# Optimization experiments

Measured on AMD Instinct MI355X. Metric: run time of the kernel, lower is better.

The kernel has to match this reference:

```python
import jax, jax.numpy as jnp
import numpy as np


def _sobel_kernels():
    # Stack the four fixed 3x3 operators into one [4,1,3,3] OIHW kernel so
    # the four single-channel convs become a single 4-output-channel conv.
    f_x = [[-1, -2, -1], [0, 0, 0], [1, 2, 1]]
    f_y = [[-1, 0, 1], [-2, 0, 2], [-1, 0, 1]]
    f_tl_br = [[-2, -1, 0], [-1, 0, 1], [0, 1, 2]]
    f_tr_bl = [[0, -1, -2], [1, 0, -1], [2, 1, 0]]
    k = np.stack([f_x, f_y, f_tl_br, f_tr_bl]).astype(np.float32)  # [4,3,3]
    return jnp.asarray(k[:, None, :, :])  # [4,1,3,3]


def setup_inputs() -> dict:
    key = jax.random.key(0)
    lab = jax.random.normal(key, (64, 1, 512, 512), dtype=jnp.float32)
    return {"lab": lab, "kernels": _sobel_kernels()}


def reference(lab, kernels):
    # lab: [B,1,H,W]; kernels: [4,1,3,3]
    lab_l = lab.astype(jnp.float32)
    taps = jax.lax.conv_general_dilated(
        lab_l, kernels,
        window_strides=(1, 1), padding=((1, 1), (1, 1)),
        dimension_numbers=("NCHW", "OIHW", "NCHW"))  # [B,4,H,W]
    edge = jnp.sum(jnp.abs(taps), axis=1)  # [B,H,W]
    # edge[edge > 0] = 1 then .long(); abs-sum is >= 0 so this is a 0/1 map
    edge = jnp.where(edge > 0, 1, 0).astype(jnp.int32)
    return edge  # squeezed: channel dim already reduced
```

## Files before the change

kernel.cpp:

```cpp
#include <hip/hip_runtime.h>


#define IMG_W 512
#define IMG_H 512
#define TROWS 16
#define SROWS (TROWS + 2)

struct Row {
  float4 lo, hi;
  float lft, rgt;
};

__device__ __forceinline__ float rget(const Row& r, int k) {
  switch (k) {
    case 0: return r.lft;
    case 1: return r.lo.x; case 2: return r.lo.y;
    case 3: return r.lo.z; case 4: return r.lo.w;
    case 5: return r.hi.x; case 6: return r.hi.y;
    case 7: return r.hi.z; case 8: return r.hi.w;
    default: return r.rgt;
  }
}

__device__ __forceinline__ void compute_store(const Row& T, const Row& M,
                                              const Row& B, int* orow) {
  int res[8];
#pragma unroll
  for (int j = 0; j < 8; ++j) {
    float t0 = rget(T, j), t1 = rget(T, j + 1), t2 = rget(T, j + 2);
    float m0 = rget(M, j),                      m2 = rget(M, j + 2);
    float b0 = rget(B, j), b1 = rget(B, j + 1), b2 = rget(B, j + 2);
    float tx = (b0 - t0) + 2.f * (b1 - t1) + (b2 - t2);
    float ty = (t2 - t0) + 2.f * (m2 - m0) + (b2 - b0);
    float d1 = -2.f * t0 - t1 - m0 + m2 + b1 + 2.f * b2;
    float d2 = -t1 - 2.f * t2 + m0 - m2 + 2.f * b0 + b1;
    float e = fabsf(tx) + fabsf(ty) + fabsf(d1) + fabsf(d2);
    res[j] = (e > 0.f) ? 1 : 0;
  }
  *reinterpret_cast<int4*>(orow)     = make_int4(res[0], res[1], res[2], res[3]);
  *reinterpret_cast<int4*>(orow + 4) = make_int4(res[4], res[5], res[6], res[7]);
}

__global__ __launch_bounds__(256) void edgenet_kernel(
    const float* __restrict__ in, int* __restrict__ out) {
  __shared__ float lds[SROWS * IMG_W];
  const int tid  = threadIdx.x;
  const int lane = tid & 63;
  const int wid  = tid >> 6;
  const int b    = blockIdx.x >> 5;
  const int t    = blockIdx.x & 31;
  const int y0   = t << 4;
  const float* img = in + (size_t)b * (IMG_H * IMG_W);

#pragma unroll
  for (int k = 0; k < 9; ++k) {
    int idx = tid + (k << 8);
    int lr  = idx >> 7;
    int c   = (idx & 127) << 2;
    int gy  = min(max(y0 + lr - 1, 0), IMG_H - 1);
    float4 v = *reinterpret_cast<const float4*>(img + gy * IMG_W + c);
    *reinterpret_cast<float4*>(&lds[lr * IMG_W + c]) = v;
  }
  __syncthreads();

  const int r0 = wid << 2;

  auto ldrow = [&](int lr, Row& r) {
    const float* p = &lds[lr * IMG_W + (lane << 3)];
    float4 lo = *reinterpret_cast<const float4*>(p);
    float4 hi = *reinterpret_cast<const float4*>(p + 4);
    float mk = ((unsigned)(y0 + lr - 1) < (unsigned)IMG_H) ? 1.f : 0.f;
    lo.x *= mk; lo.y *= mk; lo.z *= mk; lo.w *= mk;
    hi.x *= mk; hi.y *= mk; hi.z *= mk; hi.w *= mk;
    r.lo = lo; r.hi = hi;
    float lf = __shfl_up(hi.w, 1);
    float rt = __shfl_down(lo.x, 1);
    r.lft = (lane == 0)  ? 0.f : lf;
    r.rgt = (lane == 63) ? 0.f : rt;
  };

  Row s[3];
  ldrow(r0,     s[0]);
  ldrow(r0 + 1, s[1]);
  ldrow(r0 + 2, s[2]);
  int* orow = out + ((size_t)b * IMG_H + y0 + r0) * IMG_W + (lane << 3);
#pragma unroll
  for (int i = 0; i < 4; ++i) {
    compute_store(s[i % 3], s[(i + 1) % 3], s[(i + 2) % 3], orow + i * IMG_W);
    if (i < 3) ldrow(r0 + i + 3, s[i % 3]);
  }
}

extern "C" void kernel_launch(void* const* d_in, const int* in_sizes, int n_in,
                              void* d_out, int out_size, void* d_ws, size_t ws_size,
                              hipStream_t stream) {
  const float* lab = (const float*)d_in[0];
  int* out = (int*)d_out;
  int blocks = 64 * (IMG_H / TROWS);
  edgenet_kernel<<<blocks, 256, 0, stream>>>(lab, out);
}
```

Measured before the change: 28.50 us.

## Double-buffer row tiles via direct global-to-LDS loads across persistent row strips

Each block now handles a 32-row strip as four 8-row tiles. It prefetches the next tile into a second LDS buffer using global_load_lds DMA, with hand-placed vmcnt waits and barriers. This is meant to overlap global loads with stencil compute and to skip the register round-trip during staging. In exchange it adds more halo rows per output row (10 staged per 8), launches fewer blocks, and depends on fragile manual waitcnt counting and the memory ordering of the LDS writes.

```diff
diff --git a/kernel.cpp b/kernel.cpp
--- a/kernel.cpp
+++ b/kernel.cpp
@@ -1,10 +1,12 @@
 #include <hip/hip_runtime.h>
+#include <stdint.h>
 
 
 #define IMG_W 512
 #define IMG_H 512
-#define TROWS 16
-#define SROWS (TROWS + 2)
+#define TROWS 8
+#define SROWS 10
+#define NTILES 4
 
 struct Row {
   float4 lo, hi;
@@ -41,53 +43,73 @@
   *reinterpret_cast<int4*>(orow + 4) = make_int4(res[4], res[5], res[6], res[7]);
 }
 
+__device__ __forceinline__ void stage_tile(const char* img, int y0,
+                                           float* buf, int w, int lane) {
+#pragma unroll
+  for (int k = 0; k < 5; ++k) {
+    int Bo  = (k << 12) | (w << 10) | (lane << 4);
+    int row = min(max(y0 - 1 + (Bo >> 11), 0), IMG_H - 1);
+    const char* g = img + ((size_t)row << 11) + (Bo & 2047);
+    char* l = reinterpret_cast<char*>(buf) + ((k << 12) | (w << 10));
+    __builtin_amdgcn_global_load_lds(
+        (const __attribute__((address_space(1))) uint32_t*)g,
+        (__attribute__((address_space(3))) uint32_t*)l, 16, 0, 0);
+  }
+}
+
+__device__ __forceinline__ void ldrow(const float* buf, int lr, int imgrow,
+                                      int lane, Row& r) {
+  const float* p = buf + lr * IMG_W + (lane << 3);
+  float4 lo = *reinterpret_cast<const float4*>(p);
+  float4 hi = *reinterpret_cast<const float4*>(p + 4);
+  float mk = ((unsigned)imgrow < (unsigned)IMG_H) ? 1.f : 0.f;
+  lo.x *= mk; lo.y *= mk; lo.z *= mk; lo.w *= mk;
+  hi.x *= mk; hi.y *= mk; hi.z *= mk; hi.w *= mk;
+  r.lo = lo; r.hi = hi;
+  float lf = __shfl_up(hi.w, 1);
+  float rt = __shfl_down(lo.x, 1);
+  r.lft = (lane == 0)  ? 0.f : lf;
+  r.rgt = (lane == 63) ? 0.f : rt;
+}
+
 __global__ __launch_bounds__(256) void edgenet_kernel(
     const float* __restrict__ in, int* __restrict__ out) {
-  __shared__ float lds[SROWS * IMG_W];
+  __shared__ float lds[2][SROWS * IMG_W];
   const int tid  = threadIdx.x;
   const int lane = tid & 63;
-  const int wid  = tid >> 6;
-  const int b    = blockIdx.x >> 5;
-  const int t    = blockIdx.x & 31;
-  const int y0   = t << 4;
-  const float* img = in + (size_t)b * (IMG_H * IMG_W);
+  const int w    = tid >> 6;
+  const int b    = blockIdx.x >> 4;
+  const int Y0   = (blockIdx.x & 15) << 5;
+  const char* img =
+      reinterpret_cast<const char*>(in + (size_t)b * (IMG_H * IMG_W));
+
+  stage_tile(img, Y0, &lds[0][0], w, lane);
 
 #pragma unroll
-  for (int k = 0; k < 9; ++k) {
-    int idx = tid + (k << 8);
-    int lr  = idx >> 7;
-    int c   = (idx & 127) << 2;
-    int gy  = min(max(y0 + lr - 1, 0), IMG_H - 1);
-    float4 v = *reinterpret_cast<const float4*>(img + gy * IMG_W + c);
-    *reinterpret_cast<float4*>(&lds[lr * IMG_W + c]) = v;
-  }
-  __syncthreads();
+  for (int t = 0; t < NTILES; ++t) {
+    const int y0 = Y0 + t * TROWS;
+    if (t + 1 < NTILES)
+      stage_tile(img, y0 + TROWS, &lds[(t + 1) & 1][0], w, lane);
 
-  const int r0 = wid << 2;
+    if (t == 0)                asm volatile("s_waitcnt vmcnt(5)" ::: "memory");
+    else if (t < NTILES - 1)   asm volatile("s_waitcnt vmcnt(9)" ::: "memory");
+    else                       asm volatile("s_waitcnt vmcnt(4)" ::: "memory");
+    __builtin_amdgcn_sched_barrier(0);
+    __builtin_amdgcn_s_barrier();
 
-  auto ldrow = [&](int lr, Row& r) {
-    const float* p = &lds[lr * IMG_W + (lane << 3)];
-    float4 lo = *reinterpret_cast<const float4*>(p);
-    float4 hi = *reinterpret_cast<const float4*>(p + 4);
-    float mk = ((unsigned)(y0 + lr - 1) < (unsigned)IMG_H) ? 1.f : 0.f;
-    lo.x *= mk; lo.y *= mk; lo.z *= mk; lo.w *= mk;
-    hi.x *= mk; hi.y *= mk; hi.z *= mk; hi.w *= mk;
-    r.lo = lo; r.hi = hi;
-    float lf = __shfl_up(hi.w, 1);
-    float rt = __shfl_down(lo.x, 1);
-    r.lft = (lane == 0)  ? 0.f : lf;
-    r.rgt = (lane == 63) ? 0.f : rt;
-  };
+    const float* buf = &lds[t & 1][0];
+    const int r0 = w << 1;
+    Row s0, s1, s2, s3;
+    ldrow(buf, r0,     y0 - 1 + r0, lane, s0);
+    ldrow(buf, r0 + 1, y0     + r0, lane, s1);
+    ldrow(buf, r0 + 2, y0 + 1 + r0, lane, s2);
+    ldrow(buf, r0 + 3, y0 + 2 + r0, lane, s3);
+    int* orow = out + ((size_t)b * IMG_H + y0 + r0) * IMG_W + (lane << 3);
+    compute_store(s0, s1, s2, orow);
+    compute_store(s1, s2, s3, orow + IMG_W);
 
-  Row s[3];
-  ldrow(r0,     s[0]);
-  ldrow(r0 + 1, s[1]);
-  ldrow(r0 + 2, s[2]);
-  int* orow = out + ((size_t)b * IMG_H + y0 + r0) * IMG_W + (lane << 3);
-#pragma unroll
-  for (int i = 0; i < 4; ++i) {
-    compute_store(s[i % 3], s[(i + 1) % 3], s[(i + 2) % 3], orow + i * IMG_W);
-    if (i < 3) ldrow(r0 + i + 3, s[i % 3]);
+    if (t + 1 < NTILES)
+      __builtin_amdgcn_s_barrier();
   }
 }
 
@@ -96,6 +118,6 @@
                               hipStream_t stream) {
   const float* lab = (const float*)d_in[0];
   int* out = (int*)d_out;
-  int blocks = 64 * (IMG_H / TROWS);
+  int blocks = 64 * (IMG_H / (NTILES * TROWS));
   edgenet_kernel<<<blocks, 256, 0, stream>>>(lab, out);
 }
```

After: 29.27 us. +2.7%, slower.
